# Optimization experiments

Measured on AMD Instinct MI355X. Metric: run time of the kernel, lower is better.

Reference implementation:

```python
import jax, jax.numpy as jnp
import numpy as np

N_ROWS = 65536  # number of rows of the sparse input matrix


def setup_inputs() -> dict:
    key = jax.random.key(0)
    k1, k2, k3, k4, k5 = jax.random.split(key, 5)
    nnz, d_in, d_out = 524288, 512, 512
    rows = jax.random.randint(k1, (nnz,), 0, N_ROWS, dtype=jnp.int64)
    cols = jax.random.randint(k2, (nnz,), 0, d_in, dtype=jnp.int64)
    values = jax.random.normal(k3, (nnz,), dtype=jnp.float32)
    weight = jax.random.normal(k4, (d_out, d_in), dtype=jnp.float32) * (1.0 / np.sqrt(d_in))
    bound = 1.0 / np.sqrt(d_in)
    bias = jax.random.uniform(k5, (d_out,), minval=-bound, maxval=bound, dtype=jnp.float32)
    return {"rows": rows, "cols": cols, "values": values, "weight": weight, "bias": bias}


def reference(rows, cols, values, weight, bias):
    # y = sparse_input @ weight.T + bias
    # Each nonzero (r, c, v) contributes v * weight[:, c] to output row r.
    # weight: [d_out, d_in]; gather columns -> [nnz, d_out], segment-sum by row.
    contrib = values[:, None] * weight.T[cols]          # [nnz, d_out]
    y = jax.ops.segment_sum(contrib, rows, num_segments=N_ROWS)  # [N, d_out]
    return y + bias
```

## Files before the change

### kernel.cpp

```cpp
#include <hip/hip_runtime.h>
#include <hip/hip_bf16.h>

#define D 512
#define NROWS 65536
#define NBINS 256
#define RPB 256
#define P1B 1024
#define SEGCAP 16
#define MAXBLK1 512
#define BINCAP 2816
#define OVFCAP 4096

typedef float f32x4 __attribute__((ext_vector_type(4)));

__global__ __launch_bounds__(256) void k_phase1(const float* __restrict__ w,
                                                __hip_bfloat16* __restrict__ wt,
                                                const int* __restrict__ rows,
                                                const int* __restrict__ cols,
                                                const float* __restrict__ vals, int nnz, int nblk1,
                                                uint2* __restrict__ gBin, int* __restrict__ gBinCnt,
                                                int* __restrict__ ovf_cnt, uint4* __restrict__ ovf) {
    int b = blockIdx.x, t = threadIdx.x;
    if (b < 256) {
        __shared__ float tile[32][33];
        if (b == 0 && t == 0) *ovf_cnt = 0;
        int bx = b & 15, by = b >> 4;
        int tx = t & 31, ty = t >> 5;
        for (int i = ty; i < 32; i += 8)
            tile[i][tx] = w[(by * 32 + i) * D + bx * 32 + tx];
        __syncthreads();
        for (int i = ty; i < 32; i += 8)
            wt[(bx * 32 + i) * D + by * 32 + tx] = __float2bfloat16(tile[tx][i]);
        return;
    }
    __shared__ int  binCnt[NBINS];
    __shared__ uint2 binBuf[NBINS][SEGCAP];
    b -= 256;
    binCnt[t] = 0;
    __syncthreads();
    int base = b * P1B;
    int end = base + P1B; if (end > nnz) end = nnz;
    for (int i = base + t; i < end; i += 256) {
        int r = rows[i], c = cols[i];
        unsigned vb = __float_as_uint(vals[i]);
        int bin = r >> 8;
        int pos = atomicAdd(&binCnt[bin], 1);
        if (pos < SEGCAP) {
            binBuf[bin][pos] = make_uint2(((unsigned)r << 9) | (unsigned)c, vb);
        } else {
            int o = atomicAdd(ovf_cnt, 1);
            if (o < OVFCAP) ovf[o] = make_uint4((unsigned)r, (unsigned)c, vb, 0u);
        }
    }
    __syncthreads();
    for (int idx = t; idx < NBINS * SEGCAP; idx += 256) {
        int bin = idx >> 4, slot = idx & (SEGCAP - 1);
        int cnt = binCnt[bin]; if (cnt > SEGCAP) cnt = SEGCAP;
        if (slot < cnt)
            gBin[((size_t)b * NBINS + bin) * SEGCAP + slot] = binBuf[bin][slot];
        if (slot == 0) gBinCnt[b * NBINS + bin] = cnt;
    }
}

#define ACC8(wb, vv)                                   \
    do {                                               \
        f32x4 w0, w1;                                  \
        w0.x = __uint_as_float((wb).x << 16);          \
        w0.y = __uint_as_float((wb).x & 0xffff0000u);  \
        w0.z = __uint_as_float((wb).y << 16);          \
        w0.w = __uint_as_float((wb).y & 0xffff0000u);  \
        w1.x = __uint_as_float((wb).z << 16);          \
        w1.y = __uint_as_float((wb).z & 0xffff0000u);  \
        w1.z = __uint_as_float((wb).w << 16);          \
        w1.w = __uint_as_float((wb).w & 0xffff0000u);  \
        a0 += (vv) * w0;                               \
        a1 += (vv) * w1;                               \
    } while (0)

__global__ __launch_bounds__(1024) void k_binspmm(const uint2* __restrict__ gBin,
                                                  const int* __restrict__ gBinCnt, int nblk1,
                                                  const uint4* __restrict__ wt4,
                                                  const f32x4* __restrict__ bias4,
                                                  f32x4* __restrict__ out,
                                                  int* __restrict__ ovf_cnt,
                                                  const uint4* __restrict__ ovf) {
    __shared__ int segCnt[MAXBLK1], segOff[MAXBLK1], scanBuf[MAXBLK1];
    __shared__ int rowCnt[RPB], rowOff[RPB], cursor[RPB];
    __shared__ uint2 pairBuf[BINCAP];
    __shared__ uint2 csrBuf[BINCAP];
    __shared__ int totalPairs;
    int bin = blockIdx.x, t = threadIdx.x;
    int sc = (t < nblk1) ? gBinCnt[t * NBINS + bin] : 0;
    if (t < MAXBLK1) scanBuf[t] = sc;
    if (t < RPB) rowCnt[t] = 0;
    __syncthreads();
    for (int off = 1; off < MAXBLK1; off <<= 1) {
        int x = (t < MAXBLK1 && t >= off) ? scanBuf[t - off] : 0;
        __syncthreads();
        if (t < MAXBLK1) scanBuf[t] += x;
        __syncthreads();
    }
    if (t < MAXBLK1) { segOff[t] = scanBuf[t] - sc; segCnt[t] = sc; }
    if (t == MAXBLK1 - 1) totalPairs = scanBuf[MAXBLK1 - 1];
    __syncthreads();
    int total = totalPairs; if (total > BINCAP) total = BINCAP;
    for (int idx = t; idx < nblk1 * SEGCAP; idx += 1024) {
        int blk = idx >> 4, slot = idx & (SEGCAP - 1);
        if (slot < segCnt[blk]) {
            int dst = segOff[blk] + slot;
            uint2 p = gBin[((size_t)blk * NBINS + bin) * SEGCAP + slot];
            if (dst < BINCAP) {
                pairBuf[dst] = p;
            } else {
                int o = atomicAdd(ovf_cnt, 1);
                if (o < OVFCAP) ovf[o];
            }
        }
    }
    __syncthreads();
    for (int k = t; k < total; k += 1024)
        atomicAdd(&rowCnt[(pairBuf[k].x >> 9) & (RPB - 1)], 1);
    __syncthreads();
    int rc = (t < RPB) ? rowCnt[t] : 0;
    if (t < RPB) scanBuf[t] = rc;
    __syncthreads();
    for (int off = 1; off < RPB; off <<= 1) {
        int x = (t < RPB && t >= off) ? scanBuf[t - off] : 0;
        __syncthreads();
        if (t < RPB) scanBuf[t] += x;
        __syncthreads();
    }
    if (t < RPB) { rowOff[t] = scanBuf[t] - rc; cursor[t] = scanBuf[t] - rc; }
    __syncthreads();
    for (int k = t; k < total; k += 1024) {
        uint2 p = pairBuf[k];
        int r = (p.x >> 9) & (RPB - 1);
        int pos = atomicAdd(&cursor[r], 1);
        csrBuf[pos] = make_uint2(p.x & 511u, p.y);
    }
    __syncthreads();
    int wv = t >> 6, lane = t & 63;
    f32x4 bb0 = bias4[lane * 2];
    f32x4 bb1 = bias4[lane * 2 + 1];
    int novf = *ovf_cnt;
    if (novf > OVFCAP) novf = OVFCAP;
    for (int rloc = wv; rloc < RPB; rloc += 16) {
        int cnt = rowCnt[rloc], o = rowOff[rloc];
        f32x4 a0 = bb0, a1 = bb1;
        for (int s = 0; s < cnt; s += 4) {
            int i1 = (s + 1 < cnt) ? s + 1 : s;
            int i2 = (s + 2 < cnt) ? s + 2 : s;
            int i3 = (s + 3 < cnt) ? s + 3 : s;
            uint2 p0 = csrBuf[o + s];
            uint2 p1 = csrBuf[o + i1];
            uint2 p2 = csrBuf[o + i2];
            uint2 p3 = csrBuf[o + i3];
            float v0 = __uint_as_float(p0.y);
            float v1 = (s + 1 < cnt) ? __uint_as_float(p1.y) : 0.f;
            float v2 = (s + 2 < cnt) ? __uint_as_float(p2.y) : 0.f;
            float v3 = (s + 3 < cnt) ? __uint_as_float(p3.y) : 0.f;
            uint4 wb0 = wt4[(size_t)p0.x * 64 + lane];
            uint4 wb1 = wt4[(size_t)p1.x * 64 + lane];
            uint4 wb2 = wt4[(size_t)p2.x * 64 + lane];
            uint4 wb3 = wt4[(size_t)p3.x * 64 + lane];
            ACC8(wb0, v0);
            ACC8(wb1, v1);
            ACC8(wb2, v2);
            ACC8(wb3, v3);
        }
        int row = (bin << 8) + rloc;
        if (novf > 0) {
            for (int e = 0; e < novf; ++e) {
                uint4 p = ovf[e];
                if ((int)p.x == row) {
                    float v = __uint_as_float(p.z);
                    uint4 wb = wt4[(size_t)p.y * 64 + lane];
                    ACC8(wb, v);
                }
            }
        }
        f32x4* op = out + (size_t)row * (D / 4);
        op[lane * 2]     = a0;
        op[lane * 2 + 1] = a1;
    }
}

__global__ void k_init_bias(const float* __restrict__ bias, float* __restrict__ out, int total) {
    int i = blockIdx.x * blockDim.x + threadIdx.x;
    if (i < total) out[i] = bias[i & (D - 1)];
}

__global__ void k_atomic_spmm(const int* __restrict__ rows, const int* __restrict__ cols,
                              const float* __restrict__ vals, int nnz,
                              const float* __restrict__ w, float* __restrict__ out) {
    int wid = (int)((blockIdx.x * blockDim.x + threadIdx.x) >> 6);
    if (wid >= nnz) return;
    int lane = threadIdx.x & 63;
    int r = rows[wid];
    int c = cols[wid];
    float v = vals[wid];
    float* op = out + (size_t)r * D + lane * 8;
#pragma unroll
    for (int k = 0; k < 8; ++k) {
        float wv = w[(size_t)(lane * 8 + k) * D + c];
        atomicAdd(&op[k], v * wv);
    }
}

extern "C" void kernel_launch(void* const* d_in, const int* in_sizes, int n_in,
                              void* d_out, int out_size, void* d_ws, size_t ws_size,
                              hipStream_t stream) {
    const int*   rows   = (const int*)d_in[0];
    const int*   cols   = (const int*)d_in[1];
    const float* vals   = (const float*)d_in[2];
    const float* weight = (const float*)d_in[3];
    const float* bias   = (const float*)d_in[4];
    float*       out    = (float*)d_out;
    const int nnz = in_sizes[0];
    const int nblk1 = (nnz + P1B - 1) / P1B;

    char* ws = (char*)d_ws;
    size_t off = 0;
    auto alloc = [&](size_t bytes) -> void* {
        off = (off + 255) & ~(size_t)255;
        void* p = ws + off;
        off += bytes;
        return p;
    };
    __hip_bfloat16* wT = (__hip_bfloat16*)alloc((size_t)D * D * sizeof(__hip_bfloat16));
    int*   ovf_cnt = (int*)  alloc(256);
    uint4* ovf     = (uint4*)alloc((size_t)OVFCAP * sizeof(uint4));
    uint2* gBin    = (uint2*)alloc((size_t)MAXBLK1 * NBINS * SEGCAP * sizeof(uint2));
    int*   gBinCnt = (int*)  alloc((size_t)MAXBLK1 * NBINS * sizeof(int));
    const size_t need_full = off;

    if (need_full <= ws_size && nblk1 <= MAXBLK1) {
        k_phase1<<<256 + nblk1, 256, 0, stream>>>(weight, wT, rows, cols, vals, nnz, nblk1,
                                                  gBin, gBinCnt, ovf_cnt, ovf);
        k_binspmm<<<NBINS, 1024, 0, stream>>>(gBin, gBinCnt, nblk1, (const uint4*)wT,
                                              (const f32x4*)bias, (f32x4*)out, ovf_cnt, ovf);
    } else {
        k_init_bias<<<(out_size + 255) / 256, 256, 0, stream>>>(bias, out, out_size);
        k_atomic_spmm<<<((size_t)nnz * 64 + 255) / 256, 256, 0, stream>>>(rows, cols, vals, nnz, weight, out);
    }
}
```

Before: 57.80 us.

## Use smaller bins with 512-thread blocks and wave-shuffle scans

```diff
diff --git a/kernel.cpp b/kernel.cpp
--- a/kernel.cpp
+++ b/kernel.cpp
@@ -3,12 +3,12 @@
 
 #define D 512
 #define NROWS 65536
-#define NBINS 256
-#define RPB 256
+#define NBINS 512
+#define RPB 128
 #define P1B 1024
-#define SEGCAP 16
+#define SEGCAP 12
 #define MAXBLK1 512
-#define BINCAP 2816
+#define BINCAP 1408
 #define OVFCAP 4096
 
 typedef float f32x4 __attribute__((ext_vector_type(4)));
@@ -37,13 +37,14 @@
     __shared__ uint2 binBuf[NBINS][SEGCAP];
     b -= 256;
     binCnt[t] = 0;
+    binCnt[t + 256] = 0;
     __syncthreads();
     int base = b * P1B;
     int end = base + P1B; if (end > nnz) end = nnz;
     for (int i = base + t; i < end; i += 256) {
         int r = rows[i], c = cols[i];
         unsigned vb = __float_as_uint(vals[i]);
-        int bin = r >> 8;
+        int bin = r >> 7;
         int pos = atomicAdd(&binCnt[bin], 1);
         if (pos < SEGCAP) {
             binBuf[bin][pos] = make_uint2(((unsigned)r << 9) | (unsigned)c, vb);
@@ -54,7 +55,7 @@
     }
     __syncthreads();
     for (int idx = t; idx < NBINS * SEGCAP; idx += 256) {
-        int bin = idx >> 4, slot = idx & (SEGCAP - 1);
+        int bin = idx / SEGCAP, slot = idx - bin * SEGCAP;
         int cnt = binCnt[bin]; if (cnt > SEGCAP) cnt = SEGCAP;
         if (slot < cnt)
             gBin[((size_t)b * NBINS + bin) * SEGCAP + slot] = binBuf[bin][slot];
@@ -77,74 +78,82 @@
         a1 += (vv) * w1;                               \
     } while (0)
 
-__global__ __launch_bounds__(1024) void k_binspmm(const uint2* __restrict__ gBin,
-                                                  const int* __restrict__ gBinCnt, int nblk1,
-                                                  const uint4* __restrict__ wt4,
-                                                  const f32x4* __restrict__ bias4,
-                                                  f32x4* __restrict__ out,
-                                                  int* __restrict__ ovf_cnt,
-                                                  const uint4* __restrict__ ovf) {
-    __shared__ int segCnt[MAXBLK1], segOff[MAXBLK1], scanBuf[MAXBLK1];
+__global__ __launch_bounds__(512) void k_binspmm(const uint2* __restrict__ gBin,
+                                                 const int* __restrict__ gBinCnt, int nblk1,
+                                                 const uint4* __restrict__ wt4,
+                                                 const f32x4* __restrict__ bias4,
+                                                 f32x4* __restrict__ out,
+                                                 int* __restrict__ ovf_cnt,
+                                                 uint4* __restrict__ ovf) {
+    __shared__ int segCnt[MAXBLK1], segOff[MAXBLK1];
     __shared__ int rowCnt[RPB], rowOff[RPB], cursor[RPB];
+    __shared__ int wsum[8], wsum2[2];
     __shared__ uint2 pairBuf[BINCAP];
     __shared__ uint2 csrBuf[BINCAP];
-    __shared__ int totalPairs;
     int bin = blockIdx.x, t = threadIdx.x;
+    int wv = t >> 6, lane = t & 63;
     int sc = (t < nblk1) ? gBinCnt[t * NBINS + bin] : 0;
-    if (t < MAXBLK1) scanBuf[t] = sc;
+    int x = sc;
+    for (int d = 1; d < 64; d <<= 1) {
+        int y = __shfl_up(x, d, 64);
+        if (lane >= d) x += y;
+    }
+    if (lane == 63) wsum[wv] = x;
     if (t < RPB) rowCnt[t] = 0;
     __syncthreads();
-    for (int off = 1; off < MAXBLK1; off <<= 1) {
-        int x = (t < MAXBLK1 && t >= off) ? scanBuf[t - off] : 0;
-        __syncthreads();
-        if (t < MAXBLK1) scanBuf[t] += x;
-        __syncthreads();
-    }
-    if (t < MAXBLK1) { segOff[t] = scanBuf[t] - sc; segCnt[t] = sc; }
-    if (t == MAXBLK1 - 1) totalPairs = scanBuf[MAXBLK1 - 1];
-    __syncthreads();
-    int total = totalPairs; if (total > BINCAP) total = BINCAP;
-    for (int idx = t; idx < nblk1 * SEGCAP; idx += 1024) {
-        int blk = idx >> 4, slot = idx & (SEGCAP - 1);
+    int woff = 0, total = 0;
+#pragma unroll
+    for (int k = 0; k < 8; ++k) {
+        int s = wsum[k];
+        if (k < wv) woff += s;
+        total += s;
+    }
+    segOff[t] = x - sc + woff;
+    segCnt[t] = sc;
+    if (total > BINCAP) total = BINCAP;
+    __syncthreads();
+    for (int idx = t; idx < nblk1 * SEGCAP; idx += 512) {
+        int blk = idx / SEGCAP, slot = idx - blk * SEGCAP;
         if (slot < segCnt[blk]) {
             int dst = segOff[blk] + slot;
             uint2 p = gBin[((size_t)blk * NBINS + bin) * SEGCAP + slot];
             if (dst < BINCAP) {
                 pairBuf[dst] = p;
+                atomicAdd(&rowCnt[(p.x >> 9) & (RPB - 1)], 1);
             } else {
                 int o = atomicAdd(ovf_cnt, 1);
-                if (o < OVFCAP) ovf[o];
+                if (o < OVFCAP)
+                    ovf[o] = make_uint4(p.x >> 9, p.x & 511u, p.y, 0u);
             }
         }
     }
     __syncthreads();
-    for (int k = t; k < total; k += 1024)
-        atomicAdd(&rowCnt[(pairBuf[k].x >> 9) & (RPB - 1)], 1);
-    __syncthreads();
     int rc = (t < RPB) ? rowCnt[t] : 0;
-    if (t < RPB) scanBuf[t] = rc;
-    __syncthreads();
-    for (int off = 1; off < RPB; off <<= 1) {
-        int x = (t < RPB && t >= off) ? scanBuf[t - off] : 0;
-        __syncthreads();
-        if (t < RPB) scanBuf[t] += x;
-        __syncthreads();
-    }
-    if (t < RPB) { rowOff[t] = scanBuf[t] - rc; cursor[t] = scanBuf[t] - rc; }
-    __syncthreads();
-    for (int k = t; k < total; k += 1024) {
+    int rx = rc;
+    for (int d = 1; d < 64; d <<= 1) {
+        int y = __shfl_up(rx, d, 64);
+        if (lane >= d) rx += y;
+    }
+    if (t < RPB && lane == 63) wsum2[wv] = rx;
+    __syncthreads();
+    if (t < RPB) {
+        int ro = rx - rc + ((wv == 1) ? wsum2[0] : 0);
+        rowOff[t] = ro;
+        cursor[t] = ro;
+    }
+    __syncthreads();
+    for (int k = t; k < total; k += 512) {
         uint2 p = pairBuf[k];
         int r = (p.x >> 9) & (RPB - 1);
         int pos = atomicAdd(&cursor[r], 1);
         csrBuf[pos] = make_uint2(p.x & 511u, p.y);
     }
     __syncthreads();
-    int wv = t >> 6, lane = t & 63;
     f32x4 bb0 = bias4[lane * 2];
     f32x4 bb1 = bias4[lane * 2 + 1];
     int novf = *ovf_cnt;
     if (novf > OVFCAP) novf = OVFCAP;
-    for (int rloc = wv; rloc < RPB; rloc += 16) {
+    for (int rloc = wv; rloc < RPB; rloc += 8) {
         int cnt = rowCnt[rloc], o = rowOff[rloc];
         f32x4 a0 = bb0, a1 = bb1;
         for (int s = 0; s < cnt; s += 4) {
@@ -168,7 +177,7 @@
             ACC8(wb2, v2);
             ACC8(wb3, v3);
         }
-        int row = (bin << 8) + rloc;
+        int row = (bin << 7) + rloc;
         if (novf > 0) {
             for (int e = 0; e < novf; ++e) {
                 uint4 p = ovf[e];
@@ -237,8 +246,8 @@
     if (need_full <= ws_size && nblk1 <= MAXBLK1) {
         k_phase1<<<256 + nblk1, 256, 0, stream>>>(weight, wT, rows, cols, vals, nnz, nblk1,
                                                   gBin, gBinCnt, ovf_cnt, ovf);
-        k_binspmm<<<NBINS, 1024, 0, stream>>>(gBin, gBinCnt, nblk1, (const uint4*)wT,
-                                              (const f32x4*)bias, (f32x4*)out, ovf_cnt, ovf);
+        k_binspmm<<<NBINS, 512, 0, stream>>>(gBin, gBinCnt, nblk1, (const uint4*)wT,
+                                             (const f32x4*)bias, (f32x4*)out, ovf_cnt, ovf);
     } else {
         k_init_bias<<<(out_size + 255) / 256, 256, 0, stream>>>(bias, out, out_size);
         k_atomic_spmm<<<((size_t)nnz * 64 + 255) / 256, 256, 0, stream>>>(rows, cols, vals, nnz, weight, out);
```

New measurement: 60.87 us. 5.3% more time.
